# Optimization experiments

Measured on AMD Instinct MI355X. Metric: run time of the kernel, lower is better.

Reference implementation:

```python
import jax, jax.numpy as jnp
import numpy as np

B, S, E = 8, 2048, 768


def setup_inputs() -> dict:
    key = jax.random.key(0)
    ks = jax.random.split(key, 9)
    scale = 1.0 / np.sqrt(E)
    return {
        "value": jax.random.normal(ks[0], (B, S, E), jnp.float32),
        "key": jax.random.normal(ks[1], (B, S, E), jnp.float32),
        "query": jax.random.normal(ks[2], (B, S, E), jnp.float32),
        "mask": jax.random.randint(ks[3], (B, 1, S), 0, 2, jnp.int32),
        "Wv": jax.random.normal(ks[4], (E, E), jnp.float32) * scale,
        "Wk": jax.random.normal(ks[5], (E, E), jnp.float32) * scale,
        "Wq": jax.random.normal(ks[6], (E, E), jnp.float32) * scale,
        "Wo": jax.random.normal(ks[7], (E, E), jnp.float32) * scale,
        "bo": jax.random.normal(ks[8], (E,), jnp.float32) * 0.01,
    }


def reference(value, key, query, mask, Wv, Wk, Wq, Wo, bo):
    # nn.Linear: y = x @ W.T  (no bias for v/k/q)
    v = jnp.einsum('bse,oe->bso', value, Wv)
    k = jnp.einsum('bse,oe->bso', key, Wk)
    q = jnp.einsum('bse,oe->bso', query, Wq)
    inv_sqrt_e = 1.0 / jnp.sqrt(jnp.float32(E))
    # NOTE: original divides BOTH q and k by sqrt(E) -> effective 1/E scaling
    q = q * inv_sqrt_e
    k = k * inv_sqrt_e
    scores = jnp.einsum('bqe,bke->bqk', q, k)  # [B, S, S]
    scores = jnp.where(mask == 0, -jnp.inf, scores)
    attn = jax.nn.softmax(scores, axis=-1)
    out = jnp.einsum('bqk,bke->bqe', attn, v)
    out = jnp.einsum('bse,oe->bso', out, Wo) + bo
    return out
```

## Files before the change

### kernel.cpp

```cpp
#include <hip/hip_runtime.h>
#include <hip/hip_bf16.h>
#include <stdint.h>

#define E_DIM 768
#define S_LEN 2048
#define BATCH 8

typedef __attribute__((ext_vector_type(8))) short short8;
typedef __attribute__((ext_vector_type(4))) float floatx4;

__device__ __forceinline__ short f2bf(float f) {
    return __builtin_bit_cast(short, __float2bfloat16(f));
}

__device__ __forceinline__ floatx4 mfma16(short8 a, short8 b, floatx4 c) {
    return __builtin_amdgcn_mfma_f32_16x16x32_bf16(a, b, c, 0, 0, 0);
}

__device__ __forceinline__ void glds16(const short* g, short* l) {
    __builtin_amdgcn_global_load_lds(
        (const __attribute__((address_space(1))) void*)g,
        (__attribute__((address_space(3))) void*)l,
        16, 0, 0);
}

__device__ __forceinline__ void gemm_core(
    const short* __restrict__ Abase, size_t sA,
    const short* __restrict__ Bbase, size_t sB,
    int K,
    short* At, short* Bt,
    floatx4 acc[4][4])
{
    const int tid  = threadIdx.x;
    const int lane = tid & 63;
    const int wv   = tid >> 6;
    const int lm   = lane & 15, lq = lane >> 4;
    const int rl   = lane >> 3, sl = lane & 7;
    const int usw  = sl ^ rl;
    const int wm   = (wv & 1) * 64, wn = (wv >> 1) * 64;

    const short* ag = Abase + (size_t)(wv * 32 + rl) * sA + usw * 8;
    const short* bg = Bbase + (size_t)(wv * 32 + rl) * sB + usw * 8;
    short* al = At + wv * 4 * 512;
    short* bl = Bt + wv * 4 * 512;
    const size_t askip = 8 * sA, bskip = 8 * sB;

    for (int kt = 0; kt < K; kt += 64) {
#pragma unroll
        for (int c = 0; c < 4; ++c) glds16(ag + c * askip + kt, al + c * 512);
#pragma unroll
        for (int c = 0; c < 4; ++c) glds16(bg + c * bskip + kt, bl + c * 512);
        __syncthreads();

#pragma unroll
        for (int s = 0; s < 2; ++s) {
            const int u = s * 4 + lq;
            short8 af[4], bf[4];
#pragma unroll
            for (int i = 0; i < 4; ++i) {
                int r = wm + i * 16 + lm;
                af[i] = *(const short8*)&At[((r >> 3) * 64 + (r & 7) * 8 + (u ^ (r & 7))) * 8];
            }
#pragma unroll
            for (int j = 0; j < 4; ++j) {
                int r = wn + j * 16 + lm;
                bf[j] = *(const short8*)&Bt[((r >> 3) * 64 + (r & 7) * 8 + (u ^ (r & 7))) * 8];
            }
#pragma unroll
            for (int i = 0; i < 4; ++i)
#pragma unroll
                for (int j = 0; j < 4; ++j)
                    acc[i][j] = mfma16(af[i], bf[j], acc[i][j]);
        }
        __syncthreads();
    }
}

__global__ void prep(const float* __restrict__ Wv, const float* __restrict__ Wk,
                     const float* __restrict__ Wq, const float* __restrict__ Wo,
                     const float* __restrict__ query, const int* __restrict__ mask,
                     short* __restrict__ Wb, short* __restrict__ xq,
                     float* __restrict__ rowsum,
                     int* __restrict__ jidx, int* __restrict__ nv,
                     int* __restrict__ nvp)
{
    __shared__ int cnt[256];
    const int blk = blockIdx.x;
    const int t   = threadIdx.x;

    if (blk < 2304) {
        const int z = blk / 576;
        const float* src = (z == 0) ? Wv : (z == 1) ? Wk : (z == 2) ? Wq : Wo;
        const float scale = (z == 2) ? (1.0f / (float)E_DIM) : 1.0f;
        size_t i = ((size_t)(blk - z * 576) * 256 + t) * 4;
        float4 f = *(const float4*)(src + i);
        short4 h;
        h.x = f2bf(f.x * scale); h.y = f2bf(f.y * scale);
        h.z = f2bf(f.z * scale); h.w = f2bf(f.w * scale);
        *(short4*)(Wb + (size_t)z * E_DIM * E_DIM + i) = h;
    } else if (blk < 6400) {
        const int g0 = blk - 2304;
        const size_t base = (size_t)g0 * 4 * E_DIM;
#pragma unroll
        for (int p = 0; p < 3; ++p) {
            size_t i = base + ((size_t)p * 256 + t) * 4;
            float4 f = *(const float4*)(query + i);
            short4 h;
            h.x = f2bf(f.x); h.y = f2bf(f.y); h.z = f2bf(f.z); h.w = f2bf(f.w);
            *(short4*)(xq + i) = h;
        }
    } else if (blk < 6416) {
        const int g0 = blk - 6400;
        *(float4*)(rowsum + ((size_t)g0 * 256 + t) * 4) = (float4){0.f, 0.f, 0.f, 0.f};
    } else {
        const int b = blk - 6416;
        int m[8];
        int c = 0;
#pragma unroll
        for (int k = 0; k < 8; ++k) {
            m[k] = mask[b * S_LEN + t * 8 + k];
            c += (m[k] != 0);
        }
        cnt[t] = c;
        __syncthreads();
        for (int off = 1; off < 256; off <<= 1) {
            int v = (t >= off) ? cnt[t - off] : 0;
            __syncthreads();
            cnt[t] += v;
            __syncthreads();
        }
        int pos = cnt[t] - c;
        const int total = cnt[255];
#pragma unroll
        for (int k = 0; k < 8; ++k)
            if (m[k] != 0) jidx[b * S_LEN + (pos++)] = t * 8 + k;
        __syncthreads();
        for (int i = total + t; i < S_LEN; i += 256) jidx[b * S_LEN + i] = 0;
        if (t == 0) {
            nv[b] = total;
            int p = (total + 127) & ~127;
            if (p < 128) p = 128;
            nvp[b] = p;
        }
    }
}

__global__ void gather_vk(const float* __restrict__ v, const float* __restrict__ k,
                          const int* __restrict__ jidx, const int* __restrict__ nvp,
                          short* __restrict__ xv, short* __restrict__ xk) {
    const int z = blockIdx.y, b = blockIdx.z;
    const int r0 = blockIdx.x * 4;
    if (r0 >= nvp[b]) return;
    const float* src = (z == 0) ? v : k;
    short* dst = (z == 0) ? xv : xk;
    const int tid = threadIdx.x;
#pragma unroll
    for (int p = 0; p < 3; ++p) {
        int g   = p * 256 + tid;
        int row = r0 + g / 192;
        int c4  = (g % 192) * 4;
        int srow = jidx[b * S_LEN + row];
        float4 f = *(const float4*)(src + ((size_t)b * S_LEN + srow) * E_DIM + c4);
        short4 h;
        h.x = f2bf(f.x); h.y = f2bf(f.y); h.z = f2bf(f.z); h.w = f2bf(f.w);
        *(short4*)(dst + ((size_t)b * S_LEN + row) * E_DIM + c4) = h;
    }
}

__global__ __launch_bounds__(256, 3) void proj_kernel(
    const short* __restrict__ xv, const short* __restrict__ xk, const short* __restrict__ xq,
    const short* __restrict__ Wb, const int* __restrict__ nvp,
    short* __restrict__ vt, short* __restrict__ kb, short* __restrict__ qb)
{
    const int z  = blockIdx.z;
    const int mt = blockIdx.x;
    const int n0 = blockIdx.y * 128;

    int b = 0, lm0 = 0;
    const short* X;
    if (z == 2) {
        X = xq + (size_t)mt * 128 * E_DIM;
    } else {
        b   = mt >> 4;
        lm0 = (mt & 15) * 128;
        if (lm0 >= nvp[b]) return;
        X = ((z == 0) ? xv : xk) + ((size_t)b * S_LEN + lm0) * E_DIM;
    }
    const short* W = Wb + (size_t)z * E_DIM * E_DIM + (size_t)n0 * E_DIM;

    __shared__ short At[128 * 64];
    __shared__ short Bt[128 * 64];

    floatx4 acc[4][4];
#pragma unroll
    for (int i = 0; i < 4; ++i)
#pragma unroll
        for (int j = 0; j < 4; ++j) acc[i][j] = (floatx4){0.f, 0.f, 0.f, 0.f};

    gemm_core(X, E_DIM, W, E_DIM, E_DIM, At, Bt, acc);

    const int lane = threadIdx.x & 63, wv = threadIdx.x >> 6;
    const int lm = lane & 15, lq = lane >> 4;
    const int wm = (wv & 1) * 64, wn = (wv >> 1) * 64;

    if (z == 0) {
#pragma unroll
        for (int i = 0; i < 4; ++i)
#pragma unroll
            for (int r = 0; r < 4; ++r) {
                int li = lm0 + wm + i * 16 + lq * 4 + r;
#pragma unroll
                for (int j = 0; j < 4; ++j) {
                    int n = n0 + wn + j * 16 + lm;
                    vt[((size_t)b * E_DIM + n) * S_LEN + li] = f2bf(acc[i][j][r]);
                }
            }
    } else if (z == 1) {
#pragma unroll
        for (int i = 0; i < 4; ++i)
#pragma unroll
            for (int r = 0; r < 4; ++r) {
                int li = lm0 + wm + i * 16 + lq * 4 + r;
#pragma unroll
                for (int j = 0; j < 4; ++j) {
                    int n = n0 + wn + j * 16 + lm;
                    kb[((size_t)b * S_LEN + li) * E_DIM + n] = f2bf(acc[i][j][r]);
                }
            }
    } else {
#pragma unroll
        for (int i = 0; i < 4; ++i)
#pragma unroll
            for (int r = 0; r < 4; ++r) {
                int m = mt * 128 + wm + i * 16 + lq * 4 + r;
#pragma unroll
                for (int j = 0; j < 4; ++j) {
                    int n = n0 + wn + j * 16 + lm;
                    qb[(size_t)m * E_DIM + n] = f2bf(acc[i][j][r]);
                }
            }
    }
}

__global__ __launch_bounds__(256, 3) void score_kernel(
    const short* __restrict__ qb, const short* __restrict__ kb,
    const int* __restrict__ nv, const int* __restrict__ nvp,
    short* __restrict__ P, float* __restrict__ rowsum)
{
    const int b  = blockIdx.z;
    const int m0 = blockIdx.x * 128;
    const int n0 = blockIdx.y * 128;
    if (n0 >= nvp[b]) return;

    __shared__ short At[128 * 64];
    __shared__ short Bt[128 * 64];

    floatx4 acc[4][4];
#pragma unroll
    for (int i = 0; i < 4; ++i)
#pragma unroll
        for (int j = 0; j < 4; ++j) acc[i][j] = (floatx4){0.f, 0.f, 0.f, 0.f};

    gemm_core(qb + ((size_t)b * S_LEN + m0) * E_DIM, E_DIM,
              kb + ((size_t)b * S_LEN + n0) * E_DIM, E_DIM, E_DIM, At, Bt, acc);

    const int lane = threadIdx.x & 63, wv = threadIdx.x >> 6;
    const int lm = lane & 15, lq = lane >> 4;
    const int wm = (wv & 1) * 64, wn = (wv >> 1) * 64;
    const int nvb = nv[b];

    float rsum[4][4];
#pragma unroll
    for (int i = 0; i < 4; ++i)
#pragma unroll
        for (int r = 0; r < 4; ++r) rsum[i][r] = 0.f;

    const size_t Pbb = (size_t)b * S_LEN * S_LEN;
#pragma unroll
    for (int j = 0; j < 4; ++j) {
        int n = n0 + wn + j * 16 + lm;
        bool valid = n < nvb;
#pragma unroll
        for (int i = 0; i < 4; ++i) {
            int mbase = m0 + wm + i * 16 + lq * 4;
#pragma unroll
            for (int r = 0; r < 4; ++r) {
                float p = valid ? __expf(acc[i][j][r]) : 0.0f;
                rsum[i][r] += p;
                P[Pbb + (size_t)(mbase + r) * S_LEN + n] = f2bf(p);
            }
        }
    }
#pragma unroll
    for (int i = 0; i < 4; ++i)
#pragma unroll
        for (int r = 0; r < 4; ++r) {
            float v = rsum[i][r];
            v += __shfl_xor(v, 1);
            v += __shfl_xor(v, 2);
            v += __shfl_xor(v, 4);
            v += __shfl_xor(v, 8);
            if (lm == 0)
                atomicAdd(&rowsum[b * S_LEN + m0 + wm + i * 16 + lq * 4 + r], v);
        }
}

__global__ __launch_bounds__(256, 3) void pv_kernel(
    const short* __restrict__ P, const short* __restrict__ vt,
    const float* __restrict__ rowsum, const int* __restrict__ nvp,
    short* __restrict__ abuf)
{
    const int b  = blockIdx.z;
    const int m0 = blockIdx.x * 128;
    const int n0 = blockIdx.y * 128;

    __shared__ short At[128 * 64];
    __shared__ short Bt[128 * 64];

    floatx4 acc[4][4];
#pragma unroll
    for (int i = 0; i < 4; ++i)
#pragma unroll
        for (int j = 0; j < 4; ++j) acc[i][j] = (floatx4){0.f, 0.f, 0.f, 0.f};

    gemm_core(P + (size_t)b * S_LEN * S_LEN + (size_t)m0 * S_LEN, S_LEN,
              vt + ((size_t)b * E_DIM + n0) * S_LEN, S_LEN, nvp[b], At, Bt, acc);

    const int lane = threadIdx.x & 63, wv = threadIdx.x >> 6;
    const int lm = lane & 15, lq = lane >> 4;
    const int wm = (wv & 1) * 64, wn = (wv >> 1) * 64;

#pragma unroll
    for (int i = 0; i < 4; ++i) {
        int mbase = m0 + wm + i * 16 + lq * 4;
#pragma unroll
        for (int r = 0; r < 4; ++r) {
            float inv = 1.0f / rowsum[b * S_LEN + mbase + r];
            size_t ob = ((size_t)b * S_LEN + mbase + r) * E_DIM;
#pragma unroll
            for (int j = 0; j < 4; ++j) {
                int n = n0 + wn + j * 16 + lm;
                abuf[ob + n] = f2bf(acc[i][j][r] * inv);
            }
        }
    }
}

__global__ __launch_bounds__(256, 3) void out_kernel(
    const short* __restrict__ A, const short* __restrict__ W,
    const float* __restrict__ bias, float* __restrict__ Y)
{
    const int m0 = blockIdx.x * 128;
    const int n0 = blockIdx.y * 128;

    __shared__ short At[128 * 64];
    __shared__ short Bt[128 * 64];

    floatx4 acc[4][4];
#pragma unroll
    for (int i = 0; i < 4; ++i)
#pragma unroll
        for (int j = 0; j < 4; ++j) acc[i][j] = (floatx4){0.f, 0.f, 0.f, 0.f};

    gemm_core(A + (size_t)m0 * E_DIM, E_DIM, W + (size_t)n0 * E_DIM, E_DIM,
              E_DIM, At, Bt, acc);

    const int lane = threadIdx.x & 63, wv = threadIdx.x >> 6;
    const int lm = lane & 15, lq = lane >> 4;
    const int wm = (wv & 1) * 64, wn = (wv >> 1) * 64;

#pragma unroll
    for (int j = 0; j < 4; ++j) {
        int n = n0 + wn + j * 16 + lm;
        float bv = bias[n];
#pragma unroll
        for (int i = 0; i < 4; ++i)
#pragma unroll
            for (int r = 0; r < 4; ++r) {
                int m = m0 + wm + i * 16 + lq * 4 + r;
                Y[(size_t)m * E_DIM + n] = acc[i][j][r] + bv;
            }
    }
}

extern "C" void kernel_launch(void* const* d_in, const int* in_sizes, int n_in,
                              void* d_out, int out_size, void* d_ws, size_t ws_size,
                              hipStream_t stream) {
    const float* value = (const float*)d_in[0];
    const float* key   = (const float*)d_in[1];
    const float* query = (const float*)d_in[2];
    const int*   mask  = (const int*)d_in[3];
    const float* Wv    = (const float*)d_in[4];
    const float* Wk    = (const float*)d_in[5];
    const float* Wq    = (const float*)d_in[6];
    const float* Wo    = (const float*)d_in[7];
    const float* bo    = (const float*)d_in[8];
    float* out = (float*)d_out;

    const size_t WN  = (size_t)E_DIM * E_DIM;
    const size_t ACT = (size_t)BATCH * S_LEN * E_DIM;

    short* Wb  = (short*)d_ws;
    short* xv  = Wb + 4 * WN;
    short* xk  = xv + ACT;
    short* xq  = xk + ACT;
    short* vt  = xq + ACT;
    short* kb  = vt + ACT;
    short* qb  = kb + ACT;
    float* rowsum = (float*)(qb + ACT);
    int*   nv  = (int*)(rowsum + (size_t)BATCH * S_LEN);
    int*   nvp = nv + BATCH;
    int*   jidx = (int*)qb;
    short* P    = xv;
    short* abuf = qb;

    prep<<<6424, 256, 0, stream>>>(Wv, Wk, Wq, Wo, query, mask,
                                   Wb, xq, rowsum, jidx, nv, nvp);

    gather_vk<<<dim3(512, 2, 8), 256, 0, stream>>>(value, key, jidx, nvp, xv, xk);

    proj_kernel<<<dim3(128, 6, 3), 256, 0, stream>>>(xv, xk, xq, Wb, nvp,
                                                     vt, kb, qb);

    score_kernel<<<dim3(16, 16, 8), 256, 0, stream>>>(qb, kb, nv, nvp, P, rowsum);

    pv_kernel<<<dim3(16, 6, 8), 256, 0, stream>>>(P, vt, rowsum, nvp, abuf);

    out_kernel<<<dim3(128, 6), 256, 0, stream>>>(abuf, Wb + 3 * WN, bo, out);
}
```

Measured before the change: 348.6 us.

## Use 256x256 tiles with 4-stage async LDS pipeline in shared GEMM core

The shared GEMM core is rewritten to use 256x256 block tiles with 8 waves and a K-step of 32. Operands are staged through a 4-deep ring of LDS buffers via global_load_lds with explicit vmcnt waits, replacing the single-buffered load/sync/compute loop. It also raises wave priority around the MFMA block. The aim is to hide global load latency and raise per-block data reuse. In exchange, grids get much smaller (for example 8x8x8 for scores, 64x3 for the output projection, which can underfill the CUs), each block needs 128 KB of LDS, and register pressure rises.

```diff
diff --git a/kernel.cpp b/kernel.cpp
--- a/kernel.cpp
+++ b/kernel.cpp
@@ -25,55 +25,69 @@
 }
 
 __device__ __forceinline__ void gemm_core(
-    const short* __restrict__ Abase, size_t sA,
-    const short* __restrict__ Bbase, size_t sB,
-    int K,
-    short* At, short* Bt,
-    floatx4 acc[4][4])
+    const short* __restrict__ Ab, size_t sA,
+    const short* __restrict__ Bb, size_t sB,
+    int K, short* At, short* Bt,
+    floatx4 acc[8][4])
 {
     const int tid  = threadIdx.x;
     const int lane = tid & 63;
     const int wv   = tid >> 6;
     const int lm   = lane & 15, lq = lane >> 4;
-    const int rl   = lane >> 3, sl = lane & 7;
-    const int usw  = sl ^ rl;
-    const int wm   = (wv & 1) * 64, wn = (wv >> 1) * 64;
-
-    const short* ag = Abase + (size_t)(wv * 32 + rl) * sA + usw * 8;
-    const short* bg = Bbase + (size_t)(wv * 32 + rl) * sB + usw * 8;
-    short* al = At + wv * 4 * 512;
-    short* bl = Bt + wv * 4 * 512;
-    const size_t askip = 8 * sA, bskip = 8 * sB;
-
-    for (int kt = 0; kt < K; kt += 64) {
-#pragma unroll
-        for (int c = 0; c < 4; ++c) glds16(ag + c * askip + kt, al + c * 512);
-#pragma unroll
-        for (int c = 0; c < 4; ++c) glds16(bg + c * bskip + kt, bl + c * 512);
-        __syncthreads();
-
-#pragma unroll
-        for (int s = 0; s < 2; ++s) {
-            const int u = s * 4 + lq;
-            short8 af[4], bf[4];
-#pragma unroll
-            for (int i = 0; i < 4; ++i) {
-                int r = wm + i * 16 + lm;
-                af[i] = *(const short8*)&At[((r >> 3) * 64 + (r & 7) * 8 + (u ^ (r & 7))) * 8];
-            }
-#pragma unroll
-            for (int j = 0; j < 4; ++j) {
-                int r = wn + j * 16 + lm;
-                bf[j] = *(const short8*)&Bt[((r >> 3) * 64 + (r & 7) * 8 + (u ^ (r & 7))) * 8];
-            }
-#pragma unroll
-            for (int i = 0; i < 4; ++i)
-#pragma unroll
-                for (int j = 0; j < 4; ++j)
-                    acc[i][j] = mfma16(af[i], bf[j], acc[i][j]);
-        }
-        __syncthreads();
-    }
+    const int wm   = (wv >> 2) << 7;
+    const int wn   = (wv & 3) << 6;
+    const int fsw  = lq ^ ((lm >> 1) & 3);
+    const int nt   = K >> 5;
+
+    const int su   = (lane & 3) ^ ((lane >> 3) & 3);
+    const int srw  = (wv << 4) + (lane >> 2);
+    const short* aS0 = Ab + (size_t)srw * sA + su * 8;
+    const short* aS1 = aS0 + (size_t)128 * sA;
+    const short* bS0 = Bb + (size_t)srw * sB + su * 8;
+    const short* bS1 = bS0 + (size_t)128 * sB;
+    short* Alw = At + (wv << 9);
+    short* Blw = Bt + (wv << 9);
+
+#define STAGE(tt) {                                   \
+        const int b4 = ((tt) & 3) << 13;              \
+        const int kc = (tt) << 5;                     \
+        glds16(aS0 + kc, Alw + b4);                   \
+        glds16(bS0 + kc, Blw + b4);                   \
+        glds16(aS1 + kc, Alw + b4 + 4096);            \
+        glds16(bS1 + kc, Blw + b4 + 4096); }
+
+    STAGE(0) STAGE(1) STAGE(2)
+    asm volatile("s_waitcnt vmcnt(8)" ::: "memory");
+    __builtin_amdgcn_s_barrier();
+
+    for (int t = 0; t < nt; ++t) {
+        if (t + 3 < nt) STAGE(t + 3)
+
+        const short* ab = At + ((t & 3) << 13);
+        const short* bb = Bt + ((t & 3) << 13);
+        short8 af[8], bf[4];
+#pragma unroll
+        for (int i = 0; i < 8; ++i)
+            af[i] = *(const short8*)&ab[((wm + i * 16 + lm) * 4 + fsw) * 8];
+#pragma unroll
+        for (int j = 0; j < 4; ++j)
+            bf[j] = *(const short8*)&bb[((wn + j * 16 + lm) * 4 + fsw) * 8];
+
+        __builtin_amdgcn_s_setprio(1);
+#pragma unroll
+        for (int i = 0; i < 8; ++i)
+#pragma unroll
+            for (int j = 0; j < 4; ++j)
+                acc[i][j] = mfma16(af[i], bf[j], acc[i][j]);
+        __builtin_amdgcn_s_setprio(0);
+
+        const int rem = nt - 1 - t;
+        if (rem >= 3)      asm volatile("s_waitcnt vmcnt(8)" ::: "memory");
+        else if (rem == 2) asm volatile("s_waitcnt vmcnt(4)" ::: "memory");
+        else if (rem == 1) asm volatile("s_waitcnt vmcnt(0)" ::: "memory");
+        if (rem > 0) __builtin_amdgcn_s_barrier();
+    }
+#undef STAGE
 }
 
 __global__ void prep(const float* __restrict__ Wv, const float* __restrict__ Wk,
@@ -167,33 +181,33 @@
     }
 }
 
-__global__ __launch_bounds__(256, 3) void proj_kernel(
+__global__ __launch_bounds__(512, 2) void proj_kernel(
     const short* __restrict__ xv, const short* __restrict__ xk, const short* __restrict__ xq,
     const short* __restrict__ Wb, const int* __restrict__ nvp,
     short* __restrict__ vt, short* __restrict__ kb, short* __restrict__ qb)
 {
     const int z  = blockIdx.z;
     const int mt = blockIdx.x;
-    const int n0 = blockIdx.y * 128;
+    const int n0 = blockIdx.y * 256;
 
     int b = 0, lm0 = 0;
     const short* X;
     if (z == 2) {
-        X = xq + (size_t)mt * 128 * E_DIM;
+        X = xq + (size_t)mt * 256 * E_DIM;
     } else {
-        b   = mt >> 4;
-        lm0 = (mt & 15) * 128;
+        b   = mt >> 3;
+        lm0 = (mt & 7) * 256;
         if (lm0 >= nvp[b]) return;
         X = ((z == 0) ? xv : xk) + ((size_t)b * S_LEN + lm0) * E_DIM;
     }
     const short* W = Wb + (size_t)z * E_DIM * E_DIM + (size_t)n0 * E_DIM;
 
-    __shared__ short At[128 * 64];
-    __shared__ short Bt[128 * 64];
-
-    floatx4 acc[4][4];
-#pragma unroll
-    for (int i = 0; i < 4; ++i)
+    __shared__ __align__(16) short At[4 * 8192];
+    __shared__ __align__(16) short Bt[4 * 8192];
+
+    floatx4 acc[8][4];
+#pragma unroll
+    for (int i = 0; i < 8; ++i)
 #pragma unroll
         for (int j = 0; j < 4; ++j) acc[i][j] = (floatx4){0.f, 0.f, 0.f, 0.f};
 
@@ -201,11 +215,11 @@
 
     const int lane = threadIdx.x & 63, wv = threadIdx.x >> 6;
     const int lm = lane & 15, lq = lane >> 4;
-    const int wm = (wv & 1) * 64, wn = (wv >> 1) * 64;
+    const int wm = (wv >> 2) << 7, wn = (wv & 3) << 6;
 
     if (z == 0) {
 #pragma unroll
-        for (int i = 0; i < 4; ++i)
+        for (int i = 0; i < 8; ++i)
 #pragma unroll
             for (int r = 0; r < 4; ++r) {
                 int li = lm0 + wm + i * 16 + lq * 4 + r;
@@ -217,7 +231,7 @@
             }
     } else if (z == 1) {
 #pragma unroll
-        for (int i = 0; i < 4; ++i)
+        for (int i = 0; i < 8; ++i)
 #pragma unroll
             for (int r = 0; r < 4; ++r) {
                 int li = lm0 + wm + i * 16 + lq * 4 + r;
@@ -229,10 +243,10 @@
             }
     } else {
 #pragma unroll
-        for (int i = 0; i < 4; ++i)
+        for (int i = 0; i < 8; ++i)
 #pragma unroll
             for (int r = 0; r < 4; ++r) {
-                int m = mt * 128 + wm + i * 16 + lq * 4 + r;
+                int m = mt * 256 + wm + i * 16 + lq * 4 + r;
 #pragma unroll
                 for (int j = 0; j < 4; ++j) {
                     int n = n0 + wn + j * 16 + lm;
@@ -242,22 +256,22 @@
     }
 }
 
-__global__ __launch_bounds__(256, 3) void score_kernel(
+__global__ __launch_bounds__(512, 2) void score_kernel(
     const short* __restrict__ qb, const short* __restrict__ kb,
     const int* __restrict__ nv, const int* __restrict__ nvp,
     short* __restrict__ P, float* __restrict__ rowsum)
 {
     const int b  = blockIdx.z;
-    const int m0 = blockIdx.x * 128;
-    const int n0 = blockIdx.y * 128;
+    const int m0 = blockIdx.x * 256;
+    const int n0 = blockIdx.y * 256;
     if (n0 >= nvp[b]) return;
 
-    __shared__ short At[128 * 64];
-    __shared__ short Bt[128 * 64];
-
-    floatx4 acc[4][4];
-#pragma unroll
-    for (int i = 0; i < 4; ++i)
+    __shared__ __align__(16) short At[4 * 8192];
+    __shared__ __align__(16) short Bt[4 * 8192];
+
+    floatx4 acc[8][4];
+#pragma unroll
+    for (int i = 0; i < 8; ++i)
 #pragma unroll
         for (int j = 0; j < 4; ++j) acc[i][j] = (floatx4){0.f, 0.f, 0.f, 0.f};
 
@@ -266,12 +280,12 @@
 
     const int lane = threadIdx.x & 63, wv = threadIdx.x >> 6;
     const int lm = lane & 15, lq = lane >> 4;
-    const int wm = (wv & 1) * 64, wn = (wv >> 1) * 64;
+    const int wm = (wv >> 2) << 7, wn = (wv & 3) << 6;
     const int nvb = nv[b];
 
-    float rsum[4][4];
-#pragma unroll
-    for (int i = 0; i < 4; ++i)
+    float rsum[8][4];
+#pragma unroll
+    for (int i = 0; i < 8; ++i)
 #pragma unroll
         for (int r = 0; r < 4; ++r) rsum[i][r] = 0.f;
 
@@ -281,7 +295,7 @@
         int n = n0 + wn + j * 16 + lm;
         bool valid = n < nvb;
 #pragma unroll
-        for (int i = 0; i < 4; ++i) {
+        for (int i = 0; i < 8; ++i) {
             int mbase = m0 + wm + i * 16 + lq * 4;
 #pragma unroll
             for (int r = 0; r < 4; ++r) {
@@ -292,7 +306,7 @@
         }
     }
 #pragma unroll
-    for (int i = 0; i < 4; ++i)
+    for (int i = 0; i < 8; ++i)
 #pragma unroll
         for (int r = 0; r < 4; ++r) {
             float v = rsum[i][r];
@@ -305,21 +319,21 @@
         }
 }
 
-__global__ __launch_bounds__(256, 3) void pv_kernel(
+__global__ __launch_bounds__(512, 2) void pv_kernel(
     const short* __restrict__ P, const short* __restrict__ vt,
     const float* __restrict__ rowsum, const int* __restrict__ nvp,
     short* __restrict__ abuf)
 {
     const int b  = blockIdx.z;
-    const int m0 = blockIdx.x * 128;
-    const int n0 = blockIdx.y * 128;
-
-    __shared__ short At[128 * 64];
-    __shared__ short Bt[128 * 64];
-
-    floatx4 acc[4][4];
-#pragma unroll
-    for (int i = 0; i < 4; ++i)
+    const int m0 = blockIdx.x * 256;
+    const int n0 = blockIdx.y * 256;
+
+    __shared__ __align__(16) short At[4 * 8192];
+    __shared__ __align__(16) short Bt[4 * 8192];
+
+    floatx4 acc[8][4];
+#pragma unroll
+    for (int i = 0; i < 8; ++i)
 #pragma unroll
         for (int j = 0; j < 4; ++j) acc[i][j] = (floatx4){0.f, 0.f, 0.f, 0.f};
 
@@ -328,10 +342,10 @@
 
     const int lane = threadIdx.x & 63, wv = threadIdx.x >> 6;
     const int lm = lane & 15, lq = lane >> 4;
-    const int wm = (wv & 1) * 64, wn = (wv >> 1) * 64;
-
-#pragma unroll
-    for (int i = 0; i < 4; ++i) {
+    const int wm = (wv >> 2) << 7, wn = (wv & 3) << 6;
+
+#pragma unroll
+    for (int i = 0; i < 8; ++i) {
         int mbase = m0 + wm + i * 16 + lq * 4;
 #pragma unroll
         for (int r = 0; r < 4; ++r) {
@@ -346,19 +360,19 @@
     }
 }
 
-__global__ __launch_bounds__(256, 3) void out_kernel(
+__global__ __launch_bounds__(512, 2) void out_kernel(
     const short* __restrict__ A, const short* __restrict__ W,
     const float* __restrict__ bias, float* __restrict__ Y)
 {
-    const int m0 = blockIdx.x * 128;
-    const int n0 = blockIdx.y * 128;
-
-    __shared__ short At[128 * 64];
-    __shared__ short Bt[128 * 64];
-
-    floatx4 acc[4][4];
-#pragma unroll
-    for (int i = 0; i < 4; ++i)
+    const int m0 = blockIdx.x * 256;
+    const int n0 = blockIdx.y * 256;
+
+    __shared__ __align__(16) short At[4 * 8192];
+    __shared__ __align__(16) short Bt[4 * 8192];
+
+    floatx4 acc[8][4];
+#pragma unroll
+    for (int i = 0; i < 8; ++i)
 #pragma unroll
         for (int j = 0; j < 4; ++j) acc[i][j] = (floatx4){0.f, 0.f, 0.f, 0.f};
 
@@ -367,14 +381,14 @@
 
     const int lane = threadIdx.x & 63, wv = threadIdx.x >> 6;
     const int lm = lane & 15, lq = lane >> 4;
-    const int wm = (wv & 1) * 64, wn = (wv >> 1) * 64;
+    const int wm = (wv >> 2) << 7, wn = (wv & 3) << 6;
 
 #pragma unroll
     for (int j = 0; j < 4; ++j) {
         int n = n0 + wn + j * 16 + lm;
         float bv = bias[n];
 #pragma unroll
-        for (int i = 0; i < 4; ++i)
+        for (int i = 0; i < 8; ++i)
 #pragma unroll
             for (int r = 0; r < 4; ++r) {
                 int m = m0 + wm + i * 16 + lq * 4 + r;
@@ -419,12 +433,12 @@
 
     gather_vk<<<dim3(512, 2, 8), 256, 0, stream>>>(value, key, jidx, nvp, xv, xk);
 
-    proj_kernel<<<dim3(128, 6, 3), 256, 0, stream>>>(xv, xk, xq, Wb, nvp,
-                                                     vt, kb, qb);
-
-    score_kernel<<<dim3(16, 16, 8), 256, 0, stream>>>(qb, kb, nv, nvp, P, rowsum);
-
-    pv_kernel<<<dim3(16, 6, 8), 256, 0, stream>>>(P, vt, rowsum, nvp, abuf);
-
-    out_kernel<<<dim3(128, 6), 256, 0, stream>>>(abuf, Wb + 3 * WN, bo, out);
-}
+    proj_kernel<<<dim3(64, 3, 3), 512, 0, stream>>>(xv, xk, xq, Wb, nvp,
+                                                    vt, kb, qb);
+
+    score_kernel<<<dim3(8, 8, 8), 512, 0, stream>>>(qb, kb, nv, nvp, P, rowsum);
+
+    pv_kernel<<<dim3(8, 3, 8), 512, 0, stream>>>(P, vt, rowsum, nvp, abuf);
+
+    out_kernel<<<dim3(64, 3), 512, 0, stream>>>(abuf, Wb + 3 * WN, bo, out);
+}
```

Measured after the change: 445.9 us. +27.9%, slower.

## Triple-buffer GEMM core with K=32 stages and async global-to-LDS prefetch

Applied to the files above, without the earlier changes.

Replaces the single-buffered K=64 loop, which had two barriers per step, with a 3-slot ring buffer of K=32 tiles. Loads for tile t+2 are issued before computing tile t, with explicit vmcnt waits and one barrier per step. The LDS swizzle layout is changed to match the 32-wide K chunks. Shared memory rises from 32KB to 48KB per block, which may limit occupancy under launch_bounds(256,3), and K must be a multiple of 32.

```diff
diff --git a/kernel.cpp b/kernel.cpp
--- a/kernel.cpp
+++ b/kernel.cpp
@@ -28,52 +28,77 @@
     const short* __restrict__ Abase, size_t sA,
     const short* __restrict__ Bbase, size_t sB,
     int K,
-    short* At, short* Bt,
+    short* L,
     floatx4 acc[4][4])
 {
     const int tid  = threadIdx.x;
     const int lane = tid & 63;
     const int wv   = tid >> 6;
     const int lm   = lane & 15, lq = lane >> 4;
-    const int rl   = lane >> 3, sl = lane & 7;
-    const int usw  = sl ^ rl;
     const int wm   = (wv & 1) * 64, wn = (wv >> 1) * 64;
 
-    const short* ag = Abase + (size_t)(wv * 32 + rl) * sA + usw * 8;
-    const short* bg = Bbase + (size_t)(wv * 32 + rl) * sB + usw * 8;
-    short* al = At + wv * 4 * 512;
-    short* bl = Bt + wv * 4 * 512;
-    const size_t askip = 8 * sA, bskip = 8 * sB;
-
-    for (int kt = 0; kt < K; kt += 64) {
-#pragma unroll
-        for (int c = 0; c < 4; ++c) glds16(ag + c * askip + kt, al + c * 512);
-#pragma unroll
-        for (int c = 0; c < 4; ++c) glds16(bg + c * bskip + kt, bl + c * 512);
-        __syncthreads();
-
-#pragma unroll
-        for (int s = 0; s < 2; ++s) {
-            const int u = s * 4 + lq;
-            short8 af[4], bf[4];
-#pragma unroll
-            for (int i = 0; i < 4; ++i) {
-                int r = wm + i * 16 + lm;
-                af[i] = *(const short8*)&At[((r >> 3) * 64 + (r & 7) * 8 + (u ^ (r & 7))) * 8];
-            }
-#pragma unroll
-            for (int j = 0; j < 4; ++j) {
-                int r = wn + j * 16 + lm;
-                bf[j] = *(const short8*)&Bt[((r >> 3) * 64 + (r & 7) * 8 + (u ^ (r & 7))) * 8];
-            }
-#pragma unroll
-            for (int i = 0; i < 4; ++i)
-#pragma unroll
-                for (int j = 0; j < 4; ++j)
-                    acc[i][j] = mfma16(af[i], bf[j], acc[i][j]);
-        }
-        __syncthreads();
-    }
+    const int slot8 = tid & 7;
+    const int pb    = tid >> 3;
+    const int U     = slot8 ^ (pb & 7);
+    const int su    = U & 3;
+    const int sr    = pb * 2 + (U >> 2);
+
+    const short* ag = Abase + (size_t)sr * sA + su * 8;
+    const short* bg = Bbase + (size_t)sr * sB + su * 8;
+    const size_t a64 = (size_t)64 * sA, b64 = (size_t)64 * sB;
+    short* dstA = L + wv * 512;
+    short* dstB = L + 4096 + wv * 512;
+
+    const int nt = K >> 5;
+
+#define STAGE(slot, kc) {                                  \
+        short* _a = dstA + (slot) * 8192;                  \
+        short* _b = dstB + (slot) * 8192;                  \
+        glds16(ag + (kc), _a);                             \
+        glds16(ag + a64 + (kc), _a + 2048);                \
+        glds16(bg + (kc), _b);                             \
+        glds16(bg + b64 + (kc), _b + 2048); }
+
+    STAGE(0, 0)
+    STAGE(1, 32)
+    asm volatile("s_waitcnt vmcnt(4)" ::: "memory");
+    __builtin_amdgcn_s_barrier();
+
+    int rs = 0, ws = 2;
+    for (int t = 0; t < nt; ++t) {
+        if (t + 2 < nt) STAGE(ws, (t + 2) << 5)
+
+        const short* ab = L + rs * 8192;
+        const short* bb = ab + 4096;
+        short8 af[4], bf[4];
+#pragma unroll
+        for (int i = 0; i < 4; ++i) {
+            int r = wm + i * 16 + lm;
+            af[i] = *(const short8*)&ab[((r >> 1) * 8 + ((((r & 1) << 2) | lq) ^ ((r >> 1) & 7))) * 8];
+        }
+#pragma unroll
+        for (int j = 0; j < 4; ++j) {
+            int r = wn + j * 16 + lm;
+            bf[j] = *(const short8*)&bb[((r >> 1) * 8 + ((((r & 1) << 2) | lq) ^ ((r >> 1) & 7))) * 8];
+        }
+#pragma unroll
+        for (int i = 0; i < 4; ++i)
+#pragma unroll
+            for (int j = 0; j < 4; ++j)
+                acc[i][j] = mfma16(af[i], bf[j], acc[i][j]);
+
+        const int rem = nt - 1 - t;
+        if (rem >= 2) {
+            asm volatile("s_waitcnt lgkmcnt(0) vmcnt(4)" ::: "memory");
+            __builtin_amdgcn_s_barrier();
+        } else if (rem == 1) {
+            asm volatile("s_waitcnt lgkmcnt(0) vmcnt(0)" ::: "memory");
+            __builtin_amdgcn_s_barrier();
+        }
+        rs = (rs == 2) ? 0 : rs + 1;
+        ws = (ws == 2) ? 0 : ws + 1;
+    }
+#undef STAGE
 }
 
 __global__ void prep(const float* __restrict__ Wv, const float* __restrict__ Wk,
@@ -188,8 +213,7 @@
     }
     const short* W = Wb + (size_t)z * E_DIM * E_DIM + (size_t)n0 * E_DIM;
 
-    __shared__ short At[128 * 64];
-    __shared__ short Bt[128 * 64];
+    __shared__ __align__(16) short L[3 * 8192];
 
     floatx4 acc[4][4];
 #pragma unroll
@@ -197,7 +221,7 @@
 #pragma unroll
         for (int j = 0; j < 4; ++j) acc[i][j] = (floatx4){0.f, 0.f, 0.f, 0.f};
 
-    gemm_core(X, E_DIM, W, E_DIM, E_DIM, At, Bt, acc);
+    gemm_core(X, E_DIM, W, E_DIM, E_DIM, L, acc);
 
     const int lane = threadIdx.x & 63, wv = threadIdx.x >> 6;
     const int lm = lane & 15, lq = lane >> 4;
@@ -252,8 +276,7 @@
     const int n0 = blockIdx.y * 128;
     if (n0 >= nvp[b]) return;
 
-    __shared__ short At[128 * 64];
-    __shared__ short Bt[128 * 64];
+    __shared__ __align__(16) short L[3 * 8192];
 
     floatx4 acc[4][4];
 #pragma unroll
@@ -262,7 +285,7 @@
         for (int j = 0; j < 4; ++j) acc[i][j] = (floatx4){0.f, 0.f, 0.f, 0.f};
 
     gemm_core(qb + ((size_t)b * S_LEN + m0) * E_DIM, E_DIM,
-              kb + ((size_t)b * S_LEN + n0) * E_DIM, E_DIM, E_DIM, At, Bt, acc);
+              kb + ((size_t)b * S_LEN + n0) * E_DIM, E_DIM, E_DIM, L, acc);
 
     const int lane = threadIdx.x & 63, wv = threadIdx.x >> 6;
     const int lm = lane & 15, lq = lane >> 4;
@@ -314,8 +337,7 @@
     const int m0 = blockIdx.x * 128;
     const int n0 = blockIdx.y * 128;
 
-    __shared__ short At[128 * 64];
-    __shared__ short Bt[128 * 64];
+    __shared__ __align__(16) short L[3 * 8192];
 
     floatx4 acc[4][4];
 #pragma unroll
@@ -324,7 +346,7 @@
         for (int j = 0; j < 4; ++j) acc[i][j] = (floatx4){0.f, 0.f, 0.f, 0.f};
 
     gemm_core(P + (size_t)b * S_LEN * S_LEN + (size_t)m0 * S_LEN, S_LEN,
-              vt + ((size_t)b * E_DIM + n0) * S_LEN, S_LEN, nvp[b], At, Bt, acc);
+              vt + ((size_t)b * E_DIM + n0) * S_LEN, S_LEN, nvp[b], L, acc);
 
     const int lane = threadIdx.x & 63, wv = threadIdx.x >> 6;
     const int lm = lane & 15, lq = lane >> 4;
@@ -353,8 +375,7 @@
     const int m0 = blockIdx.x * 128;
     const int n0 = blockIdx.y * 128;
 
-    __shared__ short At[128 * 64];
-    __shared__ short Bt[128 * 64];
+    __shared__ __align__(16) short L[3 * 8192];
 
     floatx4 acc[4][4];
 #pragma unroll
@@ -363,7 +384,7 @@
         for (int j = 0; j < 4; ++j) acc[i][j] = (floatx4){0.f, 0.f, 0.f, 0.f};
 
     gemm_core(A + (size_t)m0 * E_DIM, E_DIM, W + (size_t)n0 * E_DIM, E_DIM,
-              E_DIM, At, Bt, acc);
+              E_DIM, L, acc);
 
     const int lane = threadIdx.x & 63, wv = threadIdx.x >> 6;
     const int lm = lane & 15, lq = lane >> 4;
```

Result: slower. 369.5 us (+6.0%).
